# Optimization experiments

Measured on AMD Instinct MI355X. Metric: run time of the kernel, lower is better.

The kernel has to match this reference:

```python
import jax, jax.numpy as jnp
import numpy as np

B, S, DM, H, NSYN = 4, 2048, 768, 12, 4
HD = DM // H  # 64
EPS = 1e-12
SCALE = float(DM / H) ** -0.5  # 1/sqrt(head_dim)


def setup_inputs() -> dict:
    key = jax.random.key(0)
    ks = jax.random.split(key, 16)
    p = 0.02
    return {
        "hidden_states": jax.random.normal(ks[0], (B, S, DM), jnp.float32),
        "attention_mask": jnp.zeros((B, 1, 1, S), jnp.float32),
        "addi_key": jax.random.normal(ks[1], (B, NSYN, S, HD), jnp.float32),
        "addi_value": jax.random.normal(ks[2], (B, NSYN, S, HD), jnp.float32),
        "Wq": jax.random.normal(ks[3], (DM, DM), jnp.float32) * p,
        "bq": jnp.zeros((DM,), jnp.float32),
        "Wk": jax.random.normal(ks[4], (DM, DM), jnp.float32) * p,
        "bk": jnp.zeros((DM,), jnp.float32),
        "Wv": jax.random.normal(ks[5], (DM, DM), jnp.float32) * p,
        "bv": jnp.zeros((DM,), jnp.float32),
        "Wo": jax.random.normal(ks[6], (DM, DM), jnp.float32) * p,
        "bo": jnp.zeros((DM,), jnp.float32),
        "ln_g": jnp.ones((DM,), jnp.float32),
        "ln_b": jnp.zeros((DM,), jnp.float32),
    }


def _heads(x):
    # [B,S,DM] -> [B,H,S,HD]
    return x.reshape(B, S, H, HD).transpose(0, 2, 1, 3)


def reference(hidden_states, attention_mask, addi_key, addi_value,
              Wq, bq, Wk, bk, Wv, bv, Wo, bo, ln_g, ln_b):
    x = hidden_states
    q = _heads(jnp.einsum('bsi,oi->bso', x, Wq) + bq)
    k = _heads(jnp.einsum('bsi,oi->bso', x, Wk) + bk)
    v = _heads(jnp.einsum('bsi,oi->bso', x, Wv) + bv)
    # additive key/value injection on first NSYN heads
    k = k.at[:, :NSYN].add(addi_key)
    v = v.at[:, :NSYN].add(addi_value)
    scores = jnp.einsum('bhqd,bhkd->bhqk', q, k) * SCALE + attention_mask
    probs = jax.nn.softmax(scores, axis=-1)
    ctx = jnp.einsum('bhqk,bhkd->bhqd', probs, v)
    ctx = ctx.transpose(0, 2, 1, 3).reshape(B, S, DM)
    out = jnp.einsum('bsi,oi->bso', ctx, Wo) + bo
    h = out + x  # residual
    mu = jnp.mean(h, axis=-1, keepdims=True)
    var = jnp.mean((h - mu) ** 2, axis=-1, keepdims=True)
    return (h - mu) * jax.lax.rsqrt(var + EPS) * ln_g + ln_b
```

## Files before the change

kernel.cpp:

```cpp
#include <hip/hip_runtime.h>


typedef __bf16 bf16;
typedef __bf16 bf16x8 __attribute__((ext_vector_type(8)));
typedef __bf16 bf16x4 __attribute__((ext_vector_type(4)));
typedef float floatx4 __attribute__((ext_vector_type(4)));
typedef unsigned int uint2v __attribute__((ext_vector_type(2)));

#define BB 4
#define SS 2048
#define DM 768
#define HH 12
#define HD 64
#define NSYN 4
#define MM (BB*SS)
#define KK DM
#define SCALE 0.125f
#define LOG2E 1.4426950408889634f
#define QSCALE (SCALE * LOG2E)

#define N_X   ((size_t)MM * DM)
#define N_W   ((size_t)DM * DM)
#define N_M   ((size_t)BB * SS)

#if __has_builtin(__builtin_amdgcn_exp2f)
#define EXP2(x) __builtin_amdgcn_exp2f(x)
#else
#define EXP2(x) exp2f(x)
#endif

#define ASYNC16(gp, lp)                                                        \
    __builtin_amdgcn_global_load_lds(                                          \
        (const __attribute__((address_space(1))) unsigned int*)(gp),           \
        (__attribute__((address_space(3))) unsigned int*)(lp), 16, 0, 0)

static __device__ __forceinline__ void pl32_swap(unsigned int& a, unsigned int& b) {
#if __has_builtin(__builtin_amdgcn_permlane32_swap)
    uint2v r = __builtin_amdgcn_permlane32_swap(a, b, false, false);
    a = r[0]; b = r[1];
#else
    asm volatile("v_permlane32_swap_b32 %0, %1" : "+v"(a), "+v"(b));
#endif
}
static __device__ __forceinline__ void pl16_swap(unsigned int& a, unsigned int& b) {
#if __has_builtin(__builtin_amdgcn_permlane16_swap)
    uint2v r = __builtin_amdgcn_permlane16_swap(a, b, false, false);
    a = r[0]; b = r[1];
#else
    asm volatile("v_permlane16_swap_b32 %0, %1" : "+v"(a), "+v"(b));
#endif
}

__global__ __launch_bounds__(256) void cvt_kernel(
    const float* __restrict__ x,
    const float* __restrict__ Wq, const float* __restrict__ Wk,
    const float* __restrict__ Wv, const float* __restrict__ Wo,
    const float* __restrict__ mask,
    bf16* __restrict__ xb,
    bf16* __restrict__ Wqb, bf16* __restrict__ Wkb,
    bf16* __restrict__ Wvb, bf16* __restrict__ Wob,
    float* __restrict__ ml2e)
{
    const size_t nx4 = N_X / 4, nw4 = N_W / 4, nm4 = N_M / 4;
    size_t i = (size_t)blockIdx.x * blockDim.x + threadIdx.x;
    if (i >= nx4 + 4 * nw4) {
        size_t off = i - nx4 - 4 * nw4;
        if (off < nm4) {
            float4 m = *(const float4*)(mask + off * 4);
            float4 o = { m.x * LOG2E, m.y * LOG2E, m.z * LOG2E, m.w * LOG2E };
            *(float4*)(ml2e + off * 4) = o;
        }
        return;
    }
    const float* src; bf16* dst; size_t off;
    if (i < nx4)                { src = x;  dst = xb;  off = i; }
    else if (i < nx4 + nw4)     { src = Wq; dst = Wqb; off = i - nx4; }
    else if (i < nx4 + 2*nw4)   { src = Wk; dst = Wkb; off = i - nx4 - nw4; }
    else if (i < nx4 + 3*nw4)   { src = Wv; dst = Wvb; off = i - nx4 - 2*nw4; }
    else                        { src = Wo; dst = Wob; off = i - nx4 - 3*nw4; }
    float4 v = *(const float4*)(src + off * 4);
    bf16x4 o = { (bf16)v.x, (bf16)v.y, (bf16)v.z, (bf16)v.w };
    *(bf16x4*)(dst + off * 4) = o;
}

template<int ORD>
__device__ __forceinline__ void gemm_mainloop64(
    const bf16* __restrict__ A, const bf16* __restrict__ Bw,
    int tileM, int tileN, bf16* As, bf16* Bs, floatx4 acc[2][4])
{
    const int tid  = threadIdx.x;
    const int lane = tid & 63;
    const int wave = tid >> 6;
    const int l15 = lane & 15, quad = lane >> 4;

    const int r0a = wave * 32 + (lane >> 2);
    const int r0b = wave * 16 + (lane >> 2);
    const int cl  = (lane & 3) ^ ((lane >> 2) & 3);
    const bf16* gA = A  + (size_t)(tileM * 128 + r0a) * KK + cl * 8;
    const bf16* gB = Bw + (size_t)(tileN *  64 + r0b) * KK + cl * 8;
    bf16* lA = As + (wave * 32) * 32;
    bf16* lB = Bs + (wave * 16) * 32;

    ASYNC16(gA,           lA);
    ASYNC16(gA + 16 * KK, lA + 16 * 32);
    ASYNC16(gB,           lB);
    __syncthreads();

    const int fpc = quad ^ (l15 & 3);
    for (int kt = 0; kt < KK / 32; ++kt) {
        const int cur = kt & 1;
        if (kt + 1 < KK / 32) {
            const int nbA = (1 - cur) * 4096;
            const int nbB = (1 - cur) * 2048;
            ASYNC16(gA + (kt + 1) * 32,           lA + nbA);
            ASYNC16(gA + (kt + 1) * 32 + 16 * KK, lA + nbA + 16 * 32);
            ASYNC16(gB + (kt + 1) * 32,           lB + nbB);
        }
        const bf16* cA = As + cur * 4096;
        const bf16* cB = Bs + cur * 2048;
        bf16x8 af[2], bfr[4];
        #pragma unroll
        for (int i = 0; i < 2; ++i)
            af[i] = *(const bf16x8*)(cA + (wave * 32 + i * 16 + l15) * 32 + fpc * 8);
        #pragma unroll
        for (int j = 0; j < 4; ++j)
            bfr[j] = *(const bf16x8*)(cB + (j * 16 + l15) * 32 + fpc * 8);
        #pragma unroll
        for (int i = 0; i < 2; ++i)
            #pragma unroll
            for (int j = 0; j < 4; ++j)
                acc[i][j] = (ORD == 0)
                    ? __builtin_amdgcn_mfma_f32_16x16x32_bf16(af[i], bfr[j], acc[i][j], 0, 0, 0)
                    : __builtin_amdgcn_mfma_f32_16x16x32_bf16(bfr[j], af[i], acc[i][j], 0, 0, 0);
        __syncthreads();
    }
}

__global__ __launch_bounds__(256) void qkv_kernel(
    const bf16* __restrict__ xb,
    const bf16* __restrict__ Wqb, const float* __restrict__ bq,
    const bf16* __restrict__ Wkb, const float* __restrict__ bk,
    const bf16* __restrict__ Wvb, const float* __restrict__ bv,
    const float* __restrict__ addi_key, const float* __restrict__ addi_value,
    bf16* __restrict__ qbuf, bf16* __restrict__ kbuf, bf16* __restrict__ vtbuf)
{
    __shared__ __align__(16) bf16 As[2 * 128 * 32];
    __shared__ __align__(16) bf16 Bs[2 * 64 * 32];
    const int u = blockIdx.x;
    const int tileM = u & 63;
    const int r     = u >> 6;
    const int tileN = r % 12;
    const int z     = r / 12;
    const bf16* W     = (z == 0) ? Wqb : (z == 1) ? Wkb : Wvb;
    const float* bias = (z == 0) ? bq  : (z == 1) ? bk  : bv;

    floatx4 acc[2][4];
    #pragma unroll
    for (int i = 0; i < 2; ++i)
        #pragma unroll
        for (int j = 0; j < 4; ++j) { floatx4 zv = {0.f, 0.f, 0.f, 0.f}; acc[i][j] = zv; }

    const int lane = threadIdx.x & 63, wave = threadIdx.x >> 6;
    const int l15 = lane & 15, quad = lane >> 4;

    if (z == 2) {
        gemm_mainloop64<0>(xb, W, tileM, tileN, As, Bs, acc);
        #pragma unroll
        for (int i = 0; i < 2; ++i) {
            const int sg0 = tileM * 128 + wave * 32 + i * 16 + quad * 4;
            const int b = sg0 >> 11, s0 = sg0 & 2047;
            #pragma unroll
            for (int j = 0; j < 4; ++j) {
                const int o = tileN * 64 + j * 16 + l15;
                const float bv_ = bias[o];
                const int h = o >> 6, d = o & 63;
                float vv[4];
                #pragma unroll
                for (int rr = 0; rr < 4; ++rr) {
                    vv[rr] = acc[i][j][rr] + bv_;
                    if (h < NSYN)
                        vv[rr] += addi_value[(((size_t)b * NSYN + h) * SS + s0 + rr) * HD + d];
                }
                bf16x4 pk = { (bf16)vv[0], (bf16)vv[1], (bf16)vv[2], (bf16)vv[3] };
                *(bf16x4*)(vtbuf + (((size_t)b * HH + h) * HD + d) * SS + s0) = pk;
            }
        }
    } else {
        gemm_mainloop64<1>(xb, W, tileM, tileN, As, Bs, acc);
        #pragma unroll
        for (int i = 0; i < 2; ++i) {
            const int sg = tileM * 128 + wave * 32 + i * 16 + l15;
            const int b = sg >> 11, s = sg & 2047;
            #pragma unroll
            for (int j = 0; j < 4; ++j) {
                const int o0 = tileN * 64 + j * 16 + quad * 4;
                const int h = o0 >> 6, d0 = o0 & 63;
                float4 b4 = *(const float4*)(bias + o0);
                float vv[4] = { acc[i][j][0] + b4.x, acc[i][j][1] + b4.y,
                                acc[i][j][2] + b4.z, acc[i][j][3] + b4.w };
                if (z == 1 && h < NSYN) {
                    float4 a4 = *(const float4*)(addi_key +
                        (((size_t)b * NSYN + h) * SS + s) * HD + d0);
                    vv[0] += a4.x; vv[1] += a4.y; vv[2] += a4.z; vv[3] += a4.w;
                }
                if (z == 0) {
                    bf16x4 pk = { (bf16)(vv[0] * QSCALE), (bf16)(vv[1] * QSCALE),
                                  (bf16)(vv[2] * QSCALE), (bf16)(vv[3] * QSCALE) };
                    *(bf16x4*)(qbuf + (((size_t)b * HH + h) * SS + s) * HD + d0) = pk;
                } else {
                    bf16x4 pk = { (bf16)vv[0], (bf16)vv[1], (bf16)vv[2], (bf16)vv[3] };
                    *(bf16x4*)(kbuf + (((size_t)b * HH + h) * SS + s) * HD + d0) = pk;
                }
            }
        }
    }
}

__global__ __launch_bounds__(256, 3) void attn_kernel(
    const bf16* __restrict__ qbuf, const bf16* __restrict__ kbuf,
    const bf16* __restrict__ vtbuf, const float* __restrict__ ml2e,
    bf16* __restrict__ ctx)
{
    __shared__ __align__(16) bf16 Ks[2 * 64 * 64];
    __shared__ __align__(16) bf16 Vt[2 * 64 * 64];

    const int u  = blockIdx.x;
    const int bh = u % 48;
    const int qt = u / 48;
    const int b  = bh / 12;
    const int h  = bh % 12;
    const size_t bhs = ((size_t)b * HH + h) * SS * HD;
    const int tid = threadIdx.x, lane = tid & 63, wave = tid >> 6;
    const int l15 = lane & 15, quad = lane >> 4;
    const int q0 = qt * 128 + wave * 32;

    const int sr  = wave * 16 + (lane >> 3);
    const int scl = (lane & 7) ^ ((lane >> 3) & 7);
    const bf16* gK = kbuf  + bhs + (size_t)sr * HD + scl * 8;
    const bf16* gV = vtbuf + bhs + (size_t)sr * SS + scl * 8;
    bf16* lK = Ks + (wave * 16) * 64;
    bf16* lV = Vt + (wave * 16) * 64;

    bf16x8 qf[2][2];
    #pragma unroll
    for (int n = 0; n < 2; ++n)
        #pragma unroll
        for (int c = 0; c < 2; ++c)
            qf[n][c] = *(const bf16x8*)(qbuf + bhs +
                (size_t)(q0 + n * 16 + l15) * HD + c * 32 + quad * 8);

    bf16x8 ones;
    #pragma unroll
    for (int e = 0; e < 8; ++e) ones[e] = (bf16)1.0f;

    floatx4 acco[2][4];
    #pragma unroll
    for (int n = 0; n < 2; ++n)
        #pragma unroll
        for (int t = 0; t < 4; ++t) { floatx4 zv = {0.f, 0.f, 0.f, 0.f}; acco[n][t] = zv; }
    floatx4 lacc[2];
    { floatx4 zv = {0.f, 0.f, 0.f, 0.f}; lacc[0] = zv; lacc[1] = zv; }

    const float* mb = ml2e + (size_t)b * SS;

    #pragma unroll
    for (int p = 0; p < 2; ++p) {
        ASYNC16(gK + (size_t)p * 8 * HD,  lK + p * 512);
        ASYNC16(gV + (size_t)p * 8 * SS,  lV + p * 512);
    }
    __syncthreads();

    for (int kt = 0; kt < SS / 64; ++kt) {
        const int cur = kt & 1;
        if (kt + 1 < SS / 64) {
            const int nb = (1 - cur) * 4096;
            #pragma unroll
            for (int p = 0; p < 2; ++p) {
                ASYNC16(gK + ((size_t)(kt + 1) * 64 + p * 8) * HD, lK + nb + p * 512);
                ASYNC16(gV + (size_t)p * 8 * SS + (kt + 1) * 64,   lV + nb + p * 512);
            }
        }
        const bf16* cK = Ks + cur * 4096;
        const bf16* cV = Vt + cur * 4096;

        floatx4 sacc[2][4];
        #pragma unroll
        for (int j = 0; j < 4; ++j) {
            float4 mk = *(const float4*)(mb + kt * 64 + j * 16 + quad * 4);
            floatx4 mv = { mk.x, mk.y, mk.z, mk.w };
            sacc[0][j] = mv;
            sacc[1][j] = mv;
        }
        __builtin_amdgcn_s_setprio(1);
        #pragma unroll
        for (int c = 0; c < 2; ++c) {
            const int pc = (4 * c + quad) ^ (l15 & 7);
            #pragma unroll
            for (int j = 0; j < 4; ++j) {
                bf16x8 af = *(const bf16x8*)(cK + (j * 16 + l15) * 64 + pc * 8);
                #pragma unroll
                for (int n = 0; n < 2; ++n)
                    sacc[n][j] = __builtin_amdgcn_mfma_f32_16x16x32_bf16(af, qf[n][c], sacc[n][j], 0, 0, 0);
            }
        }
        __builtin_amdgcn_s_setprio(0);

        unsigned int w[2][4][2];
        #pragma unroll
        for (int j = 0; j < 4; ++j) {
            #pragma unroll
            for (int n = 0; n < 2; ++n) {
                float p0 = EXP2(sacc[n][j][0]);
                float p1 = EXP2(sacc[n][j][1]);
                float p2 = EXP2(sacc[n][j][2]);
                float p3 = EXP2(sacc[n][j][3]);
                union { bf16x4 v; unsigned int u2[2]; } pk;
                pk.v = (bf16x4){ (bf16)p0, (bf16)p1, (bf16)p2, (bf16)p3 };
                w[n][j][0] = pk.u2[0];
                w[n][j][1] = pk.u2[1];
            }
        }
        #pragma unroll
        for (int n = 0; n < 2; ++n) {
            pl32_swap(w[n][0][0], w[n][1][0]);  pl32_swap(w[n][0][1], w[n][1][1]);
            pl32_swap(w[n][2][0], w[n][3][0]);  pl32_swap(w[n][2][1], w[n][3][1]);
        }
        #pragma unroll
        for (int n = 0; n < 2; ++n) {
            pl16_swap(w[n][0][0], w[n][1][0]);  pl16_swap(w[n][0][1], w[n][1][1]);
            pl16_swap(w[n][2][0], w[n][3][0]);  pl16_swap(w[n][2][1], w[n][3][1]);
        }
        union { unsigned int u2[4]; bf16x8 v; } pb[2][2];
        #pragma unroll
        for (int n = 0; n < 2; ++n) {
            pb[n][0].u2[0] = w[n][0][0]; pb[n][0].u2[1] = w[n][0][1];
            pb[n][0].u2[2] = w[n][1][0]; pb[n][0].u2[3] = w[n][1][1];
            pb[n][1].u2[0] = w[n][2][0]; pb[n][1].u2[1] = w[n][2][1];
            pb[n][1].u2[2] = w[n][3][0]; pb[n][1].u2[3] = w[n][3][1];
        }

        __builtin_amdgcn_s_setprio(1);
        #pragma unroll
        for (int c = 0; c < 2; ++c) {
            const int pc = (4 * c + quad) ^ (l15 & 7);
            #pragma unroll
            for (int n = 0; n < 2; ++n)
                lacc[n] = __builtin_amdgcn_mfma_f32_16x16x32_bf16(ones, pb[n][c].v, lacc[n], 0, 0, 0);
            #pragma unroll
            for (int t = 0; t < 4; ++t) {
                bf16x8 af = *(const bf16x8*)(cV + (t * 16 + l15) * 64 + pc * 8);
                #pragma unroll
                for (int n = 0; n < 2; ++n)
                    acco[n][t] = __builtin_amdgcn_mfma_f32_16x16x32_bf16(af, pb[n][c].v, acco[n][t], 0, 0, 0);
            }
        }
        __builtin_amdgcn_s_setprio(0);
        __syncthreads();
    }

    #pragma unroll
    for (int n = 0; n < 2; ++n) {
        const float inv = 1.0f / lacc[n][0];
        bf16* crow = ctx + ((size_t)(b * SS + q0 + n * 16 + l15)) * DM + h * HD;
        #pragma unroll
        for (int t = 0; t < 4; ++t) {
            bf16x4 ov = { (bf16)(acco[n][t][0] * inv), (bf16)(acco[n][t][1] * inv),
                          (bf16)(acco[n][t][2] * inv), (bf16)(acco[n][t][3] * inv) };
            *(bf16x4*)(crow + t * 16 + quad * 4) = ov;
        }
    }
}

__global__ __launch_bounds__(256) void oproj_kernel(
    const bf16* __restrict__ ctx, const bf16* __restrict__ Wob,
    const float* __restrict__ bo, const float* __restrict__ x,
    bf16* __restrict__ hbuf)
{
    __shared__ __align__(16) bf16 As[2 * 128 * 32];
    __shared__ __align__(16) bf16 Bs[2 * 64 * 32];
    const int u = blockIdx.x;
    const int tileM = u & 63;
    const int tileN = u >> 6;

    floatx4 acc[2][4];
    #pragma unroll
    for (int i = 0; i < 2; ++i)
        #pragma unroll
        for (int j = 0; j < 4; ++j) { floatx4 zv = {0.f, 0.f, 0.f, 0.f}; acc[i][j] = zv; }

    gemm_mainloop64<1>(ctx, Wob, tileM, tileN, As, Bs, acc);

    const int lane = threadIdx.x & 63, wave = threadIdx.x >> 6;
    const int l15 = lane & 15, quad = lane >> 4;
    #pragma unroll
    for (int i = 0; i < 2; ++i) {
        const int sg = tileM * 128 + wave * 32 + i * 16 + l15;
        #pragma unroll
        for (int j = 0; j < 4; ++j) {
            const int o0 = tileN * 64 + j * 16 + quad * 4;
            float4 b4 = *(const float4*)(bo + o0);
            float4 r4 = *(const float4*)(x + (size_t)sg * DM + o0);
            bf16x4 pk = { (bf16)(acc[i][j][0] + b4.x + r4.x),
                          (bf16)(acc[i][j][1] + b4.y + r4.y),
                          (bf16)(acc[i][j][2] + b4.z + r4.z),
                          (bf16)(acc[i][j][3] + b4.w + r4.w) };
            *(bf16x4*)(hbuf + (size_t)sg * DM + o0) = pk;
        }
    }
}

__global__ __launch_bounds__(256) void ln_kernel(
    const bf16* __restrict__ hbuf, const float* __restrict__ g,
    const float* __restrict__ be, float* __restrict__ out)
{
    const int row  = blockIdx.x * 4 + (threadIdx.x >> 6);
    const int lane = threadIdx.x & 63;
    const bf16* hr = hbuf + (size_t)row * DM;

    bf16x8 va = *(const bf16x8*)(hr + lane * 8);
    bf16x4 vb = *(const bf16x4*)(hr + 512 + lane * 4);
    float v[12];
    #pragma unroll
    for (int i = 0; i < 8; ++i) v[i] = (float)va[i];
    #pragma unroll
    for (int i = 0; i < 4; ++i) v[8 + i] = (float)vb[i];

    float s = 0.f;
    #pragma unroll
    for (int i = 0; i < 12; ++i) s += v[i];
    #pragma unroll
    for (int m = 1; m < 64; m <<= 1) s += __shfl_xor(s, m);
    const float mu = s * (1.0f / DM);

    float s2 = 0.f;
    #pragma unroll
    for (int i = 0; i < 12; ++i) { v[i] -= mu; s2 += v[i] * v[i]; }
    #pragma unroll
    for (int m = 1; m < 64; m <<= 1) s2 += __shfl_xor(s2, m);
    const float rsv = rsqrtf(s2 * (1.0f / DM) + 1e-12f);

    float* orow = out + (size_t)row * DM;
    const int c0 = lane * 8, c1 = 512 + lane * 4;
    float4 g0 = *(const float4*)(g + c0),     g1 = *(const float4*)(g + c0 + 4);
    float4 g2 = *(const float4*)(g + c1);
    float4 b0 = *(const float4*)(be + c0),    b1 = *(const float4*)(be + c0 + 4);
    float4 b2 = *(const float4*)(be + c1);
    float4 o0 = { v[0]*rsv*g0.x + b0.x, v[1]*rsv*g0.y + b0.y,
                  v[2]*rsv*g0.z + b0.z, v[3]*rsv*g0.w + b0.w };
    float4 o1 = { v[4]*rsv*g1.x + b1.x, v[5]*rsv*g1.y + b1.y,
                  v[6]*rsv*g1.z + b1.z, v[7]*rsv*g1.w + b1.w };
    float4 o2 = { v[8]*rsv*g2.x + b2.x, v[9]*rsv*g2.y + b2.y,
                  v[10]*rsv*g2.z + b2.z, v[11]*rsv*g2.w + b2.w };
    *(float4*)(orow + c0)     = o0;
    *(float4*)(orow + c0 + 4) = o1;
    *(float4*)(orow + c1)     = o2;
}

extern "C" void kernel_launch(void* const* d_in, const int* in_sizes, int n_in,
                              void* d_out, int out_size, void* d_ws, size_t ws_size,
                              hipStream_t stream)
{
    const float* x    = (const float*)d_in[0];
    const float* mask = (const float*)d_in[1];
    const float* akey = (const float*)d_in[2];
    const float* aval = (const float*)d_in[3];
    const float* Wq = (const float*)d_in[4];  const float* bq = (const float*)d_in[5];
    const float* Wk = (const float*)d_in[6];  const float* bk = (const float*)d_in[7];
    const float* Wv = (const float*)d_in[8];  const float* bv = (const float*)d_in[9];
    const float* Wo = (const float*)d_in[10]; const float* bo = (const float*)d_in[11];
    const float* lng = (const float*)d_in[12]; const float* lnb = (const float*)d_in[13];
    float* outp = (float*)d_out;

    const size_t nqkv = (size_t)BB * HH * SS * HD;
    char* ws = (char*)d_ws;
    bf16*  xb   = (bf16*)ws;   ws += N_X  * sizeof(bf16);
    bf16*  Wqb  = (bf16*)ws;   ws += N_W  * sizeof(bf16);
    bf16*  Wkb  = (bf16*)ws;   ws += N_W  * sizeof(bf16);
    bf16*  Wvb  = (bf16*)ws;   ws += N_W  * sizeof(bf16);
    bf16*  Wob  = (bf16*)ws;   ws += N_W  * sizeof(bf16);
    float* ml2e = (float*)ws;  ws += N_M  * sizeof(float);
    bf16*  qbuf = (bf16*)ws;   ws += nqkv * sizeof(bf16);
    bf16*  kbuf = (bf16*)ws;   ws += nqkv * sizeof(bf16);
    bf16*  vtbuf= (bf16*)ws;   ws += nqkv * sizeof(bf16);
    bf16*  ctxb = (bf16*)ws;   ws += nqkv * sizeof(bf16);
    bf16*  hbuf = (bf16*)ws;   ws += nqkv * sizeof(bf16);

    const size_t ncvt = (N_X + 4 * N_W + N_M) / 4;
    const int cvt_blocks = (int)((ncvt + 255) / 256);
    cvt_kernel<<<cvt_blocks, 256, 0, stream>>>(x, Wq, Wk, Wv, Wo, mask,
                                               xb, Wqb, Wkb, Wvb, Wob, ml2e);

    qkv_kernel<<<2304, 256, 0, stream>>>(xb, Wqb, bq, Wkb, bk, Wvb, bv, akey, aval,
                                         qbuf, kbuf, vtbuf);
    attn_kernel<<<768, 256, 0, stream>>>(qbuf, kbuf, vtbuf, ml2e, ctxb);
    oproj_kernel<<<768, 256, 0, stream>>>(ctxb, Wob, bo, x, hbuf);
    ln_kernel<<<MM / 4, 256, 0, stream>>>(hbuf, lng, lnb, outp);
}
```

Before: 266.2 us.

## Widen QKV GEMM tile to 128x128 and strengthen LDS swizzle

The QKV projection kernel now computes a 128x128 output tile per block instead of 128x64, halving the block count and reusing each A-fragment across eight B fragments. This is meant to cut redundant global/LDS traffic for the activation matrix. The LDS XOR swizzle is also extended with an extra term to reduce bank conflicts, and launch bounds request 4 blocks per CU. In exchange it uses more accumulator registers and twice the B shared memory, which may lower occupancy and produce fewer blocks for load balancing.

Result: no change. 268.8 us (+1.0%).

```diff
diff --git a/kernel.cpp b/kernel.cpp
--- a/kernel.cpp
+++ b/kernel.cpp
@@ -83,6 +83,9 @@
     *(bf16x4*)(dst + off * 4) = o;
 }
 
+#define STG_CL(lane)  (((lane) & 3) ^ (((lane) >> 2) & 3) ^ (((lane) >> 4) & 3))
+#define FRG_PC(quad, l15)  ((quad) ^ ((l15) & 3) ^ (((l15) >> 2) & 3))
+
 template<int ORD>
 __device__ __forceinline__ void gemm_mainloop64(
     const bf16* __restrict__ A, const bf16* __restrict__ Bw,
@@ -95,7 +98,7 @@
 
     const int r0a = wave * 32 + (lane >> 2);
     const int r0b = wave * 16 + (lane >> 2);
-    const int cl  = (lane & 3) ^ ((lane >> 2) & 3);
+    const int cl  = STG_CL(lane);
     const bf16* gA = A  + (size_t)(tileM * 128 + r0a) * KK + cl * 8;
     const bf16* gB = Bw + (size_t)(tileN *  64 + r0b) * KK + cl * 8;
     bf16* lA = As + (wave * 32) * 32;
@@ -106,7 +109,7 @@
     ASYNC16(gB,           lB);
     __syncthreads();
 
-    const int fpc = quad ^ (l15 & 3);
+    const int fpc = FRG_PC(quad, l15);
     for (int kt = 0; kt < KK / 32; ++kt) {
         const int cur = kt & 1;
         if (kt + 1 < KK / 32) {
@@ -136,7 +139,59 @@
     }
 }
 
-__global__ __launch_bounds__(256) void qkv_kernel(
+template<int ORD>
+__device__ __forceinline__ void gemm_mainloop128(
+    const bf16* __restrict__ A, const bf16* __restrict__ Bw,
+    int tileM, bf16* As, bf16* Bs, floatx4 acc[2][8])
+{
+    const int tid  = threadIdx.x;
+    const int lane = tid & 63;
+    const int wave = tid >> 6;
+    const int l15 = lane & 15, quad = lane >> 4;
+
+    const int r0 = wave * 32 + (lane >> 2);
+    const int cl = STG_CL(lane);
+    const bf16* gA = A  + (size_t)(tileM * 128 + r0) * KK + cl * 8;
+    const bf16* gB = Bw + (size_t)r0 * KK + cl * 8;
+    bf16* lA = As + (wave * 32) * 32;
+    bf16* lB = Bs + (wave * 32) * 32;
+
+    ASYNC16(gA,           lA);
+    ASYNC16(gA + 16 * KK, lA + 16 * 32);
+    ASYNC16(gB,           lB);
+    ASYNC16(gB + 16 * KK, lB + 16 * 32);
+    __syncthreads();
+
+    const int fpc = FRG_PC(quad, l15);
+    for (int kt = 0; kt < KK / 32; ++kt) {
+        const int cur = kt & 1;
+        if (kt + 1 < KK / 32) {
+            const int nb = (1 - cur) * 4096;
+            ASYNC16(gA + (kt + 1) * 32,           lA + nb);
+            ASYNC16(gA + (kt + 1) * 32 + 16 * KK, lA + nb + 16 * 32);
+            ASYNC16(gB + (kt + 1) * 32,           lB + nb);
+            ASYNC16(gB + (kt + 1) * 32 + 16 * KK, lB + nb + 16 * 32);
+        }
+        const bf16* cA = As + cur * 4096;
+        const bf16* cB = Bs + cur * 4096;
+        bf16x8 af[2];
+        #pragma unroll
+        for (int i = 0; i < 2; ++i)
+            af[i] = *(const bf16x8*)(cA + (wave * 32 + i * 16 + l15) * 32 + fpc * 8);
+        #pragma unroll
+        for (int j = 0; j < 8; ++j) {
+            bf16x8 bfr = *(const bf16x8*)(cB + (j * 16 + l15) * 32 + fpc * 8);
+            #pragma unroll
+            for (int i = 0; i < 2; ++i)
+                acc[i][j] = (ORD == 0)
+                    ? __builtin_amdgcn_mfma_f32_16x16x32_bf16(af[i], bfr, acc[i][j], 0, 0, 0)
+                    : __builtin_amdgcn_mfma_f32_16x16x32_bf16(bfr, af[i], acc[i][j], 0, 0, 0);
+        }
+        __syncthreads();
+    }
+}
+
+__global__ __launch_bounds__(256, 4) void qkv_kernel(
     const bf16* __restrict__ xb,
     const bf16* __restrict__ Wqb, const float* __restrict__ bq,
     const bf16* __restrict__ Wkb, const float* __restrict__ bk,
@@ -145,33 +200,34 @@
     bf16* __restrict__ qbuf, bf16* __restrict__ kbuf, bf16* __restrict__ vtbuf)
 {
     __shared__ __align__(16) bf16 As[2 * 128 * 32];
-    __shared__ __align__(16) bf16 Bs[2 * 64 * 32];
+    __shared__ __align__(16) bf16 Bs[2 * 128 * 32];
     const int u = blockIdx.x;
     const int tileM = u & 63;
-    const int r     = u >> 6;
-    const int tileN = r % 12;
-    const int z     = r / 12;
+    const int tileN = u >> 6;
+    const int z     = tileN / 6;
+    const int tN    = tileN % 6;
     const bf16* W     = (z == 0) ? Wqb : (z == 1) ? Wkb : Wvb;
     const float* bias = (z == 0) ? bq  : (z == 1) ? bk  : bv;
-
-    floatx4 acc[2][4];
+    const bf16* Wrow  = W + (size_t)(tN * 128) * KK;
+
+    floatx4 acc[2][8];
     #pragma unroll
     for (int i = 0; i < 2; ++i)
         #pragma unroll
-        for (int j = 0; j < 4; ++j) { floatx4 zv = {0.f, 0.f, 0.f, 0.f}; acc[i][j] = zv; }
+        for (int j = 0; j < 8; ++j) { floatx4 zv = {0.f, 0.f, 0.f, 0.f}; acc[i][j] = zv; }
 
     const int lane = threadIdx.x & 63, wave = threadIdx.x >> 6;
     const int l15 = lane & 15, quad = lane >> 4;
 
     if (z == 2) {
-        gemm_mainloop64<0>(xb, W, tileM, tileN, As, Bs, acc);
+        gemm_mainloop128<0>(xb, Wrow, tileM, As, Bs, acc);
         #pragma unroll
         for (int i = 0; i < 2; ++i) {
             const int sg0 = tileM * 128 + wave * 32 + i * 16 + quad * 4;
             const int b = sg0 >> 11, s0 = sg0 & 2047;
             #pragma unroll
-            for (int j = 0; j < 4; ++j) {
-                const int o = tileN * 64 + j * 16 + l15;
+            for (int j = 0; j < 8; ++j) {
+                const int o = tN * 128 + j * 16 + l15;
                 const float bv_ = bias[o];
                 const int h = o >> 6, d = o & 63;
                 float vv[4];
@@ -186,14 +242,14 @@
             }
         }
     } else {
-        gemm_mainloop64<1>(xb, W, tileM, tileN, As, Bs, acc);
+        gemm_mainloop128<1>(xb, Wrow, tileM, As, Bs, acc);
         #pragma unroll
         for (int i = 0; i < 2; ++i) {
             const int sg = tileM * 128 + wave * 32 + i * 16 + l15;
             const int b = sg >> 11, s = sg & 2047;
             #pragma unroll
-            for (int j = 0; j < 4; ++j) {
-                const int o0 = tileN * 64 + j * 16 + quad * 4;
+            for (int j = 0; j < 8; ++j) {
+                const int o0 = tN * 128 + j * 16 + quad * 4;
                 const int h = o0 >> 6, d0 = o0 & 63;
                 float4 b4 = *(const float4*)(bias + o0);
                 float vv[4] = { acc[i][j][0] + b4.x, acc[i][j][1] + b4.y,
@@ -490,7 +546,7 @@
     cvt_kernel<<<cvt_blocks, 256, 0, stream>>>(x, Wq, Wk, Wv, Wo, mask,
                                                xb, Wqb, Wkb, Wvb, Wob, ml2e);
 
-    qkv_kernel<<<2304, 256, 0, stream>>>(xb, Wqb, bq, Wkb, bk, Wvb, bv, akey, aval,
+    qkv_kernel<<<1152, 256, 0, stream>>>(xb, Wqb, bq, Wkb, bk, Wvb, bv, akey, aval,
                                          qbuf, kbuf, vtbuf);
     attn_kernel<<<768, 256, 0, stream>>>(qbuf, kbuf, vtbuf, ml2e, ctxb);
     oproj_kernel<<<768, 256, 0, stream>>>(ctxb, Wob, bo, x, hbuf);
```

## Enlarge GEMM tiles to 256x128 with wider LDS swizzle and hoist mask loads

Applied to the files above, without the earlier changes.

The QKV and output-projection GEMMs move from 128x64 block tiles to 256x128 tiles. Each wave now computes a 64x128 sub-tile with a 4x8 accumulator array, which raises arithmetic intensity and reuse of fragments loaded from LDS. The LDS swizzle is widened to three XOR terms to reduce bank conflicts, and the grid sizes shrink to 576 and 192 blocks. Separately, the attention kernel loads the mask at the start of each key-tile iteration so that load latency is hidden earlier. The trade-off is many more registers per thread and fewer blocks; 192 blocks for oproj is below the CU count, which risks leaving compute units idle.

New measurement: 306.9 us. 15.3% more time.

```diff
diff --git a/kernel.cpp b/kernel.cpp
--- a/kernel.cpp
+++ b/kernel.cpp
@@ -83,60 +83,66 @@
     *(bf16x4*)(dst + off * 4) = o;
 }
 
+#define STG_CL(lane)  (((lane) & 3) ^ (((lane) >> 2) & 3) ^ (((lane) >> 4) & 3))
+#define FRG_PC(quad, l15)  ((quad) ^ ((l15) & 3) ^ (((l15) >> 2) & 3))
+
 template<int ORD>
-__device__ __forceinline__ void gemm_mainloop64(
+__device__ __forceinline__ void gemm_mainloop256(
     const bf16* __restrict__ A, const bf16* __restrict__ Bw,
-    int tileM, int tileN, bf16* As, bf16* Bs, floatx4 acc[2][4])
+    int tileM, bf16* As, bf16* Bs, floatx4 acc[4][8])
 {
     const int tid  = threadIdx.x;
     const int lane = tid & 63;
     const int wave = tid >> 6;
     const int l15 = lane & 15, quad = lane >> 4;
 
-    const int r0a = wave * 32 + (lane >> 2);
-    const int r0b = wave * 16 + (lane >> 2);
-    const int cl  = (lane & 3) ^ ((lane >> 2) & 3);
-    const bf16* gA = A  + (size_t)(tileM * 128 + r0a) * KK + cl * 8;
-    const bf16* gB = Bw + (size_t)(tileN *  64 + r0b) * KK + cl * 8;
-    bf16* lA = As + (wave * 32) * 32;
-    bf16* lB = Bs + (wave * 16) * 32;
-
-    ASYNC16(gA,           lA);
-    ASYNC16(gA + 16 * KK, lA + 16 * 32);
-    ASYNC16(gB,           lB);
+    const int rA = wave * 64 + (lane >> 2);
+    const int rB = wave * 32 + (lane >> 2);
+    const int cl = STG_CL(lane);
+    const bf16* gA = A  + (size_t)(tileM * 256 + rA) * KK + cl * 8;
+    const bf16* gB = Bw + (size_t)rB * KK + cl * 8;
+    bf16* lA = As + (wave * 64) * 32;
+    bf16* lB = Bs + (wave * 32) * 32;
+
+    #pragma unroll
+    for (int g = 0; g < 4; ++g) ASYNC16(gA + (size_t)g * 16 * KK, lA + g * 512);
+    #pragma unroll
+    for (int g = 0; g < 2; ++g) ASYNC16(gB + (size_t)g * 16 * KK, lB + g * 512);
     __syncthreads();
 
-    const int fpc = quad ^ (l15 & 3);
+    const int fpc = FRG_PC(quad, l15);
     for (int kt = 0; kt < KK / 32; ++kt) {
         const int cur = kt & 1;
         if (kt + 1 < KK / 32) {
-            const int nbA = (1 - cur) * 4096;
-            const int nbB = (1 - cur) * 2048;
-            ASYNC16(gA + (kt + 1) * 32,           lA + nbA);
-            ASYNC16(gA + (kt + 1) * 32 + 16 * KK, lA + nbA + 16 * 32);
-            ASYNC16(gB + (kt + 1) * 32,           lB + nbB);
-        }
-        const bf16* cA = As + cur * 4096;
-        const bf16* cB = Bs + cur * 2048;
-        bf16x8 af[2], bfr[4];
-        #pragma unroll
-        for (int i = 0; i < 2; ++i)
-            af[i] = *(const bf16x8*)(cA + (wave * 32 + i * 16 + l15) * 32 + fpc * 8);
-        #pragma unroll
-        for (int j = 0; j < 4; ++j)
-            bfr[j] = *(const bf16x8*)(cB + (j * 16 + l15) * 32 + fpc * 8);
-        #pragma unroll
-        for (int i = 0; i < 2; ++i)
-            #pragma unroll
-            for (int j = 0; j < 4; ++j)
+            const int nbA = (1 - cur) * 8192;
+            const int nbB = (1 - cur) * 4096;
+            #pragma unroll
+            for (int g = 0; g < 4; ++g)
+                ASYNC16(gA + (kt + 1) * 32 + (size_t)g * 16 * KK, lA + nbA + g * 512);
+            #pragma unroll
+            for (int g = 0; g < 2; ++g)
+                ASYNC16(gB + (kt + 1) * 32 + (size_t)g * 16 * KK, lB + nbB + g * 512);
+        }
+        const bf16* cA = As + cur * 8192;
+        const bf16* cB = Bs + cur * 4096;
+        bf16x8 af[4];
+        #pragma unroll
+        for (int i = 0; i < 4; ++i)
+            af[i] = *(const bf16x8*)(cA + (wave * 64 + i * 16 + l15) * 32 + fpc * 8);
+        #pragma unroll
+        for (int j = 0; j < 8; ++j) {
+            bf16x8 bfr = *(const bf16x8*)(cB + (j * 16 + l15) * 32 + fpc * 8);
+            #pragma unroll
+            for (int i = 0; i < 4; ++i)
                 acc[i][j] = (ORD == 0)
-                    ? __builtin_amdgcn_mfma_f32_16x16x32_bf16(af[i], bfr[j], acc[i][j], 0, 0, 0)
-                    : __builtin_amdgcn_mfma_f32_16x16x32_bf16(bfr[j], af[i], acc[i][j], 0, 0, 0);
+                    ? __builtin_amdgcn_mfma_f32_16x16x32_bf16(af[i], bfr, acc[i][j], 0, 0, 0)
+                    : __builtin_amdgcn_mfma_f32_16x16x32_bf16(bfr, af[i], acc[i][j], 0, 0, 0);
+        }
         __syncthreads();
     }
 }
 
-__global__ __launch_bounds__(256) void qkv_kernel(
+__global__ __launch_bounds__(256, 2) void qkv_kernel(
     const bf16* __restrict__ xb,
     const bf16* __restrict__ Wqb, const float* __restrict__ bq,
     const bf16* __restrict__ Wkb, const float* __restrict__ bk,
@@ -144,34 +150,35 @@
     const float* __restrict__ addi_key, const float* __restrict__ addi_value,
     bf16* __restrict__ qbuf, bf16* __restrict__ kbuf, bf16* __restrict__ vtbuf)
 {
-    __shared__ __align__(16) bf16 As[2 * 128 * 32];
-    __shared__ __align__(16) bf16 Bs[2 * 64 * 32];
+    __shared__ __align__(16) bf16 As[2 * 256 * 32];
+    __shared__ __align__(16) bf16 Bs[2 * 128 * 32];
     const int u = blockIdx.x;
-    const int tileM = u & 63;
-    const int r     = u >> 6;
-    const int tileN = r % 12;
-    const int z     = r / 12;
+    const int tileM = u & 31;
+    const int tileN = u >> 5;
+    const int z     = tileN / 6;
+    const int tN    = tileN % 6;
     const bf16* W     = (z == 0) ? Wqb : (z == 1) ? Wkb : Wvb;
     const float* bias = (z == 0) ? bq  : (z == 1) ? bk  : bv;
-
-    floatx4 acc[2][4];
-    #pragma unroll
-    for (int i = 0; i < 2; ++i)
-        #pragma unroll
-        for (int j = 0; j < 4; ++j) { floatx4 zv = {0.f, 0.f, 0.f, 0.f}; acc[i][j] = zv; }
+    const bf16* Wrow  = W + (size_t)(tN * 128) * KK;
+
+    floatx4 acc[4][8];
+    #pragma unroll
+    for (int i = 0; i < 4; ++i)
+        #pragma unroll
+        for (int j = 0; j < 8; ++j) { floatx4 zv = {0.f, 0.f, 0.f, 0.f}; acc[i][j] = zv; }
 
     const int lane = threadIdx.x & 63, wave = threadIdx.x >> 6;
     const int l15 = lane & 15, quad = lane >> 4;
 
     if (z == 2) {
-        gemm_mainloop64<0>(xb, W, tileM, tileN, As, Bs, acc);
-        #pragma unroll
-        for (int i = 0; i < 2; ++i) {
-            const int sg0 = tileM * 128 + wave * 32 + i * 16 + quad * 4;
+        gemm_mainloop256<0>(xb, Wrow, tileM, As, Bs, acc);
+        #pragma unroll
+        for (int i = 0; i < 4; ++i) {
+            const int sg0 = tileM * 256 + wave * 64 + i * 16 + quad * 4;
             const int b = sg0 >> 11, s0 = sg0 & 2047;
             #pragma unroll
-            for (int j = 0; j < 4; ++j) {
-                const int o = tileN * 64 + j * 16 + l15;
+            for (int j = 0; j < 8; ++j) {
+                const int o = tN * 128 + j * 16 + l15;
                 const float bv_ = bias[o];
                 const int h = o >> 6, d = o & 63;
                 float vv[4];
@@ -186,14 +193,14 @@
             }
         }
     } else {
-        gemm_mainloop64<1>(xb, W, tileM, tileN, As, Bs, acc);
-        #pragma unroll
-        for (int i = 0; i < 2; ++i) {
-            const int sg = tileM * 128 + wave * 32 + i * 16 + l15;
+        gemm_mainloop256<1>(xb, Wrow, tileM, As, Bs, acc);
+        #pragma unroll
+        for (int i = 0; i < 4; ++i) {
+            const int sg = tileM * 256 + wave * 64 + i * 16 + l15;
             const int b = sg >> 11, s = sg & 2047;
             #pragma unroll
-            for (int j = 0; j < 4; ++j) {
-                const int o0 = tileN * 64 + j * 16 + quad * 4;
+            for (int j = 0; j < 8; ++j) {
+                const int o0 = tN * 128 + j * 16 + quad * 4;
                 const int h = o0 >> 6, d0 = o0 & 63;
                 float4 b4 = *(const float4*)(bias + o0);
                 float vv[4] = { acc[i][j][0] + b4.x, acc[i][j][1] + b4.y,
@@ -271,6 +278,11 @@
     __syncthreads();
 
     for (int kt = 0; kt < SS / 64; ++kt) {
+        float4 mk4[4];
+        #pragma unroll
+        for (int j = 0; j < 4; ++j)
+            mk4[j] = *(const float4*)(mb + kt * 64 + j * 16 + quad * 4);
+
         const int cur = kt & 1;
         if (kt + 1 < SS / 64) {
             const int nb = (1 - cur) * 4096;
@@ -286,8 +298,7 @@
         floatx4 sacc[2][4];
         #pragma unroll
         for (int j = 0; j < 4; ++j) {
-            float4 mk = *(const float4*)(mb + kt * 64 + j * 16 + quad * 4);
-            floatx4 mv = { mk.x, mk.y, mk.z, mk.w };
+            floatx4 mv = { mk4[j].x, mk4[j].y, mk4[j].z, mk4[j].w };
             sacc[0][j] = mv;
             sacc[1][j] = mv;
         }
@@ -371,33 +382,34 @@
     }
 }
 
-__global__ __launch_bounds__(256) void oproj_kernel(
+__global__ __launch_bounds__(256, 2) void oproj_kernel(
     const bf16* __restrict__ ctx, const bf16* __restrict__ Wob,
     const float* __restrict__ bo, const float* __restrict__ x,
     bf16* __restrict__ hbuf)
 {
-    __shared__ __align__(16) bf16 As[2 * 128 * 32];
-    __shared__ __align__(16) bf16 Bs[2 * 64 * 32];
+    __shared__ __align__(16) bf16 As[2 * 256 * 32];
+    __shared__ __align__(16) bf16 Bs[2 * 128 * 32];
     const int u = blockIdx.x;
-    const int tileM = u & 63;
-    const int tileN = u >> 6;
-
-    floatx4 acc[2][4];
-    #pragma unroll
-    for (int i = 0; i < 2; ++i)
-        #pragma unroll
-        for (int j = 0; j < 4; ++j) { floatx4 zv = {0.f, 0.f, 0.f, 0.f}; acc[i][j] = zv; }
-
-    gemm_mainloop64<1>(ctx, Wob, tileM, tileN, As, Bs, acc);
+    const int tileM = u & 31;
+    const int tileN = u >> 5;
+    const bf16* Wrow = Wob + (size_t)(tileN * 128) * KK;
+
+    floatx4 acc[4][8];
+    #pragma unroll
+    for (int i = 0; i < 4; ++i)
+        #pragma unroll
+        for (int j = 0; j < 8; ++j) { floatx4 zv = {0.f, 0.f, 0.f, 0.f}; acc[i][j] = zv; }
+
+    gemm_mainloop256<1>(ctx, Wrow, tileM, As, Bs, acc);
 
     const int lane = threadIdx.x & 63, wave = threadIdx.x >> 6;
     const int l15 = lane & 15, quad = lane >> 4;
     #pragma unroll
-    for (int i = 0; i < 2; ++i) {
-        const int sg = tileM * 128 + wave * 32 + i * 16 + l15;
-        #pragma unroll
-        for (int j = 0; j < 4; ++j) {
-            const int o0 = tileN * 64 + j * 16 + quad * 4;
+    for (int i = 0; i < 4; ++i) {
+        const int sg = tileM * 256 + wave * 64 + i * 16 + l15;
+        #pragma unroll
+        for (int j = 0; j < 8; ++j) {
+            const int o0 = tileN * 128 + j * 16 + quad * 4;
             float4 b4 = *(const float4*)(bo + o0);
             float4 r4 = *(const float4*)(x + (size_t)sg * DM + o0);
             bf16x4 pk = { (bf16)(acc[i][j][0] + b4.x + r4.x),
@@ -490,9 +502,9 @@
     cvt_kernel<<<cvt_blocks, 256, 0, stream>>>(x, Wq, Wk, Wv, Wo, mask,
                                                xb, Wqb, Wkb, Wvb, Wob, ml2e);
 
-    qkv_kernel<<<2304, 256, 0, stream>>>(xb, Wqb, bq, Wkb, bk, Wvb, bv, akey, aval,
-                                         qbuf, kbuf, vtbuf);
+    qkv_kernel<<<576, 256, 0, stream>>>(xb, Wqb, bq, Wkb, bk, Wvb, bv, akey, aval,
+                                        qbuf, kbuf, vtbuf);
     attn_kernel<<<768, 256, 0, stream>>>(qbuf, kbuf, vtbuf, ml2e, ctxb);
-    oproj_kernel<<<768, 256, 0, stream>>>(ctxb, Wob, bo, x, hbuf);
+    oproj_kernel<<<192, 256, 0, stream>>>(ctxb, Wob, bo, x, hbuf);
     ln_kernel<<<MM / 4, 256, 0, stream>>>(hbuf, lng, lnb, outp);
 }
```
